# Kernel tuning notes

Hardware: AMD Instinct MI355X
Metric: run time of the kernel (lower is better)

The kernel has to match this reference:

```python
import jax, jax.numpy as jnp
import numpy as np

K = 3          # kernel_size
STRIDE_H = 1
STRIDE_W = 1


def setup_inputs() -> dict:
    key = jax.random.key(0)
    k1, k2, k3, k4 = jax.random.split(key, 4)
    inputs = jax.random.normal(k1, (8, 128, 128, 128), dtype=jnp.float32)
    weight = jax.random.normal(k2, (128, 128, K, K), dtype=jnp.float32) * 0.05
    # learned per-image rate map, fractional dilations in [1, 3)
    rates = jax.random.uniform(k3, (1, 1, 32, 32), dtype=jnp.float32) * 2.0 + 1.0
    bias = jax.random.normal(k4, (128,), dtype=jnp.float32) * 0.01
    return {"inputs": inputs, "weight": weight, "rates": rates, "bias": bias}


def _interp_bilinear(r, out_h, out_w):
    # torch F.interpolate(mode='bilinear', align_corners=False) on a 2D map r[in_h,in_w]
    in_h, in_w = r.shape
    def src(n_out, n_in):
        s = (jnp.arange(n_out, dtype=jnp.float32) + 0.5) * (n_in / n_out) - 0.5
        return jnp.clip(s, 0.0, n_in - 1.0)
    sy = src(out_h, in_h)
    sx = src(out_w, in_w)
    y0 = jnp.floor(sy).astype(jnp.int32)
    x0 = jnp.floor(sx).astype(jnp.int32)
    y1 = jnp.minimum(y0 + 1, in_h - 1)
    x1 = jnp.minimum(x0 + 1, in_w - 1)
    wy = (sy - y0.astype(jnp.float32))[:, None]   # [out_h,1]
    wx = (sx - x0.astype(jnp.float32))[None, :]   # [1,out_w]
    return (r[y0[:, None], x0[None, :]] * (1 - wy) * (1 - wx)
            + r[y0[:, None], x1[None, :]] * (1 - wy) * wx
            + r[y1[:, None], x0[None, :]] * wy * (1 - wx)
            + r[y1[:, None], x1[None, :]] * wy * wx)


def _bilinear_sample(img, y, x):
    # img: [N,C,H,W]; y,x: [Ho,Wo] float positions; zero padding outside.
    H, W = img.shape[2], img.shape[3]
    y0 = jnp.floor(y).astype(jnp.int32)
    x0 = jnp.floor(x).astype(jnp.int32)
    y1, x1 = y0 + 1, x0 + 1
    wy = y - y0.astype(img.dtype)
    wx = x - x0.astype(img.dtype)
    def tap(yi, xi):
        m = ((yi >= 0) & (yi < H) & (xi >= 0) & (xi < W)).astype(img.dtype)
        yc = jnp.clip(yi, 0, H - 1)
        xc = jnp.clip(xi, 0, W - 1)
        return img[:, :, yc, xc] * m  # [N,C,Ho,Wo]
    return (tap(y0, x0) * (1 - wy) * (1 - wx)
            + tap(y0, x1) * (1 - wy) * wx
            + tap(y1, x0) * wy * (1 - wx)
            + tap(y1, x1) * wy * wx)


def reference(inputs, weight, rates, bias):
    N, Cin, H, W = inputs.shape
    Ho = (H - K) // STRIDE_H + 1
    Wo = (W - K) // STRIDE_W + 1
    rate = _interp_bilinear(rates[0, 0], Ho, Wo)          # [Ho,Wo]
    base_y = jnp.arange(Ho, dtype=jnp.float32)[:, None] * STRIDE_H
    base_x = jnp.arange(Wo, dtype=jnp.float32)[None, :] * STRIDE_W
    out = jnp.broadcast_to(bias[None, :, None, None], (N, weight.shape[0], Ho, Wo)).astype(inputs.dtype)
    # fixed K*K = 9 taps; each tap samples the input at p0 + k*rate (per-pixel dilation)
    for kh in range(K):
        for kw in range(K):
            y = base_y + kh * rate
            x = base_x + kw * rate
            samp = _bilinear_sample(inputs, y, x)          # [N,Cin,Ho,Wo]
            out = out + jnp.einsum('oc,nchw->nohw', weight[:, :, kh, kw], samp)
    return out
```

## Files before the change

### kernel.cpp

```cpp
#include <hip/hip_runtime.h>
#include <hip/hip_fp16.h>

#define N_    8
#define CIN   128
#define COUT  128
#define H_    128
#define W_    128
#define HO    126
#define WO    126
#define PIXPER (HO*WO)
#define TOTPIX (N_*PIXPER)
#define PT    128
#define BLKPERIMG 125
#define NBLK  (N_*BLKPERIMG)

typedef _Float16 f16x8 __attribute__((ext_vector_type(8)));
typedef _Float16 f16x4 __attribute__((ext_vector_type(4)));
typedef float    f32x4 __attribute__((ext_vector_type(4)));

union U4H {
    uint4   u;
    __half2 h[4];
    f16x8   f;
};

#define GLLDS(gp, lp) __builtin_amdgcn_global_load_lds( \
    (const __attribute__((address_space(1))) unsigned int*)(gp), \
    (__attribute__((address_space(3))) unsigned int*)(lp), 16, 0, 0)

__global__ __launch_bounds__(256) void transpose_in_kernel(
    const float* __restrict__ in, _Float16* __restrict__ in_cl)
{
    __shared__ float tile[64][65];
    int bid = blockIdx.x;
    int hwt = bid & 255;
    int ct  = (bid >> 8) & 1;
    int n   = bid >> 9;
    int r0  = threadIdx.x >> 4;
    int c4  = (threadIdx.x & 15) * 4;
    const float* src = in + ((size_t)(n * CIN + ct * 64) * 16384) + hwt * 64;
#pragma unroll
    for (int k = 0; k < 4; ++k) {
        int row = r0 + k * 16;
        float4 v = *(const float4*)(src + (size_t)row * 16384 + c4);
        *(float4*)&tile[row][c4] = v;
    }
    __syncthreads();
    _Float16* dst = in_cl + ((size_t)(n * 16384 + hwt * 64) * 128) + ct * 64;
#pragma unroll
    for (int k = 0; k < 4; ++k) {
        int hw = r0 + k * 16;
        f16x4 o;
        o[0] = (_Float16)tile[c4 + 0][hw];
        o[1] = (_Float16)tile[c4 + 1][hw];
        o[2] = (_Float16)tile[c4 + 2][hw];
        o[3] = (_Float16)tile[c4 + 3][hw];
        *(f16x4*)(dst + (size_t)hw * 128 + c4) = o;
    }
}

__global__ void transpose_w_kernel(const float* __restrict__ w, _Float16* __restrict__ wt) {
    int t = blockIdx.x * 256 + threadIdx.x;
    int o = t >> 7, c = t & 127;
    int g = c >> 3;
    int dst = (((o << 4) | (g ^ (o & 7))) << 3) | (c & 7);
    const float* s = w + (size_t)(o * 128 + c) * 9;
#pragma unroll
    for (int tap = 0; tap < 9; ++tap)
        wt[tap * 16384 + dst] = (_Float16)s[tap];
}

__device__ __forceinline__ void gather_issue(
    int KH, int KW, U4H (&G)[4][4], int j0, int grp, int gl, unsigned nbase,
    const _Float16* __restrict__ in_cl,
    const int (*sPYi)[PT], const int (*sPXi)[PT])
{
    const unsigned lo = (unsigned)(gl * 8);
#pragma unroll
    for (int jj = 0; jj < 4; ++jj) {
        int px = grp * 8 + j0 + jj;
        int y0 = sPYi[KH][px];
        int x0 = sPXi[KW][px];
        int yc0 = min(y0, H_ - 1), yc1 = min(y0 + 1, H_ - 1);
        int xc0 = min(x0, W_ - 1), xc1 = min(x0 + 1, W_ - 1);
        G[jj][0].u = *(const uint4*)(in_cl + (((nbase + (unsigned)(yc0 * W_ + xc0)) << 7) + lo));
        if (KW != 0)
            G[jj][1].u = *(const uint4*)(in_cl + (((nbase + (unsigned)(yc0 * W_ + xc1)) << 7) + lo));
        if (KH != 0)
            G[jj][2].u = *(const uint4*)(in_cl + (((nbase + (unsigned)(yc1 * W_ + xc0)) << 7) + lo));
        if (KH != 0 && KW != 0)
            G[jj][3].u = *(const uint4*)(in_cl + (((nbase + (unsigned)(yc1 * W_ + xc1)) << 7) + lo));
    }
}

__device__ __forceinline__ void gather_lerp_store(
    int KH, int KW, U4H (&G)[4][4], int j0, int grp, int gl,
    _Float16* sS,
    const int (*sPYi)[PT], const float (*sPYf)[PT],
    const int (*sPXi)[PT], const float (*sPXf)[PT])
{
#pragma unroll
    for (int jj = 0; jj < 4; ++jj) {
        int j  = j0 + jj;
        int px = grp * 8 + j;
        U4H S;
        if (KH == 0 && KW == 0) {
            S = G[jj][0];
        } else {
            int   y0 = sPYi[KH][px];  float wy = sPYf[KH][px];
            int   x0 = sPXi[KW][px];  float wx = sPXf[KW][px];
            float vy0 = (y0 <= H_ - 1) ? 1.0f : 0.0f;
            float vy1 = (y0 <= H_ - 2) ? 1.0f : 0.0f;
            float vx0 = (x0 <= W_ - 1) ? 1.0f : 0.0f;
            float vx1 = (x0 <= W_ - 2) ? 1.0f : 0.0f;
            __half2 w00 = __float2half2_rn((1.0f - wy) * (1.0f - wx) * vy0 * vx0);
            __half2 w01 = __float2half2_rn((1.0f - wy) * wx * vy0 * vx1);
            __half2 w10 = __float2half2_rn(wy * (1.0f - wx) * vy1 * vx0);
            __half2 w11 = __float2half2_rn(wy * wx * vy1 * vx1);
#pragma unroll
            for (int d = 0; d < 4; ++d) {
                __half2 s = __hmul2(G[jj][0].h[d], w00);
                if (KW != 0)              s = __hfma2(G[jj][1].h[d], w01, s);
                if (KH != 0)              s = __hfma2(G[jj][2].h[d], w10, s);
                if (KH != 0 && KW != 0)   s = __hfma2(G[jj][3].h[d], w11, s);
                S.h[d] = s;
            }
        }
        *(f16x8*)&sS[px * 128 + ((unsigned)(gl ^ j)) * 8] = S.f;
    }
}

__global__ __launch_bounds__(256, 2) void adc_main(
    const _Float16* __restrict__ in_cl, const _Float16* __restrict__ wt,
    const float* __restrict__ rates, const float* __restrict__ bias,
    float* __restrict__ out)
{
    __shared__ uint4    sW[2048];
    __shared__ __align__(16) _Float16 sS[PT * 128];
    __shared__ int      sPYi[3][PT];
    __shared__ float    sPYf[3][PT];
    __shared__ int      sPXi[3][PT];
    __shared__ float    sPXf[3][PT];

    const int t    = threadIdx.x;
    const int lane = t & 63;
    const int wv   = t >> 6;
    const int l15  = lane & 15;
    const int quad = lane >> 4;

    const int n     = blockIdx.x & 7;
    const int pbase = (blockIdx.x >> 3) * PT;
    const unsigned nbase = (unsigned)n << 14;

    if (t < PT) {
        int rem = min(pbase + t, PIXPER - 1);
        int ho = rem / WO, wo = rem - ho * WO;
        const float sc = 32.0f / 126.0f;
        float sy = fminf(fmaxf(((float)ho + 0.5f) * sc - 0.5f, 0.0f), 31.0f);
        float sx = fminf(fmaxf(((float)wo + 0.5f) * sc - 0.5f, 0.0f), 31.0f);
        int y0 = (int)sy, x0 = (int)sx;
        int y1 = min(y0 + 1, 31), x1 = min(x0 + 1, 31);
        float wy = sy - (float)y0, wx = sx - (float)x0;
        float r = rates[y0 * 32 + x0] * (1.0f - wy) * (1.0f - wx)
                + rates[y0 * 32 + x1] * (1.0f - wy) * wx
                + rates[y1 * 32 + x0] * wy * (1.0f - wx)
                + rates[y1 * 32 + x1] * wy * wx;
#pragma unroll
        for (int k = 0; k < 3; ++k) {
            float fy  = (float)ho + (float)k * r;
            float fy0 = floorf(fy);
            sPYi[k][t] = (int)fy0;
            sPYf[k][t] = fy - fy0;
            float fx  = (float)wo + (float)k * r;
            float fx0 = floorf(fx);
            sPXi[k][t] = (int)fx0;
            sPXf[k][t] = fx - fx0;
        }
    }

    f32x4 acc[8][2];
    const f32x4 zero = {0.0f, 0.0f, 0.0f, 0.0f};
#pragma unroll
    for (int i = 0; i < 8; ++i) { acc[i][0] = zero; acc[i][1] = zero; }

    const int grp = t >> 4;
    const int gl  = t & 15;

    __syncthreads();

    U4H G[4][4];

    gather_issue(0, 0, G, 0, grp, gl, nbase, in_cl, sPYi, sPXi);

#pragma unroll
    for (int tap = 0; tap < 9; ++tap) {
        const int kh = tap / 3;
        const int kw = tap - kh * 3;

        const uint4* wsrc = (const uint4*)(wt + tap * 16384);
#pragma unroll
        for (int i = 0; i < 8; ++i) {
            int base = i * 256 + (wv << 6);
            GLLDS(wsrc + base + lane, &sW[base]);
        }

        gather_lerp_store(kh, kw, G, 0, grp, gl, sS, sPYi, sPYf, sPXi, sPXf);
        gather_issue(kh, kw, G, 4, grp, gl, nbase, in_cl, sPYi, sPXi);
        gather_lerp_store(kh, kw, G, 4, grp, gl, sS, sPYi, sPYf, sPXi, sPXf);

        __syncthreads();

        if (tap < 8) {
            const int tap1 = tap + 1;
            const int kh1 = tap1 / 3;
            const int kw1 = tap1 - kh1 * 3;
            gather_issue(kh1, kw1, G, 0, grp, gl, nbase, in_cl, sPYi, sPXi);
        }

#pragma unroll
        for (int ks = 0; ks < 4; ++ks) {
            const int g  = (ks << 2) | quad;
            const int sw = g ^ (l15 & 7);
            f16x8 b0 = *(const f16x8*)&sS[(wv * 32 +      l15) * 128 + sw * 8];
            f16x8 b1 = *(const f16x8*)&sS[(wv * 32 + 16 + l15) * 128 + sw * 8];
#pragma unroll
            for (int mt = 0; mt < 8; ++mt) {
                int o = (mt << 4) | l15;
                U4H AF;
                AF.u = sW[(o << 4) | sw];
                acc[mt][0] = __builtin_amdgcn_mfma_f32_16x16x32_f16(AF.f, b0, acc[mt][0], 0, 0, 0);
                acc[mt][1] = __builtin_amdgcn_mfma_f32_16x16x32_f16(AF.f, b1, acc[mt][1], 0, 0, 0);
            }
        }
        __syncthreads();
    }

#pragma unroll
    for (int pt = 0; pt < 2; ++pt) {
        int p    = (wv << 5) + (pt << 4) + l15;
        int prel = pbase + p;
        int rem2 = min(prel, PIXPER - 1);
        float* obase = out + (size_t)n * (COUT * PIXPER) + rem2;
        if (prel < PIXPER) {
#pragma unroll
            for (int mt = 0; mt < 8; ++mt) {
                int o0 = (mt << 4) + (quad << 2);
                float4 bs = *(const float4*)(bias + o0);
                f32x4 a0 = acc[mt][pt];
                obase[(size_t)(o0 + 0) * PIXPER] = a0[0] + bs.x;
                obase[(size_t)(o0 + 1) * PIXPER] = a0[1] + bs.y;
                obase[(size_t)(o0 + 2) * PIXPER] = a0[2] + bs.z;
                obase[(size_t)(o0 + 3) * PIXPER] = a0[3] + bs.w;
            }
        }
    }
}

extern "C" void kernel_launch(void* const* d_in, const int* in_sizes, int n_in,
                              void* d_out, int out_size, void* d_ws, size_t ws_size,
                              hipStream_t stream) {
    const float* inputs = (const float*)d_in[0];
    const float* weight = (const float*)d_in[1];
    const float* rates  = (const float*)d_in[2];
    const float* bias   = (const float*)d_in[3];
    float* out = (float*)d_out;

    char* ws = (char*)d_ws;
    _Float16* in_cl = (_Float16*)ws;
    _Float16* wtp   = (_Float16*)(ws + 33554432);

    transpose_w_kernel<<<64, 256, 0, stream>>>(weight, wtp);
    transpose_in_kernel<<<4096, 256, 0, stream>>>(inputs, in_cl);
    adc_main<<<NBLK, 256, 0, stream>>>(in_cl, wtp, rates, bias, out);
}
```

Before: 186.3 us.

## Read MFMA weights from global in fragment layout and precompute bilinear tap weights

Drops the per-tap LDS staging of weights. The weights are pre-permuted so each lane's MFMA A fragment is one contiguous 16-byte global load served from cache. The bilinear corner weights for all 9 taps are precomputed once per pixel as packed halves in shared memory, which removes the per-tap float math. Freeing LDS and registers raises launch_bounds occupancy to 3 blocks per CU. In exchange, the cross-tap gather prefetch is removed, so gather latency is now exposed, and weight reads go through L1/L2 on every MFMA step.

```diff
diff --git a/kernel.cpp b/kernel.cpp
--- a/kernel.cpp
+++ b/kernel.cpp
@@ -23,10 +23,10 @@
     __half2 h[4];
     f16x8   f;
 };
-
-#define GLLDS(gp, lp) __builtin_amdgcn_global_load_lds( \
-    (const __attribute__((address_space(1))) unsigned int*)(gp), \
-    (__attribute__((address_space(3))) unsigned int*)(lp), 16, 0, 0)
+union U2H {
+    uint2  u;
+    __half h[4];
+};
 
 __global__ __launch_bounds__(256) void transpose_in_kernel(
     const float* __restrict__ in, _Float16* __restrict__ in_cl)
@@ -62,12 +62,15 @@
 __global__ void transpose_w_kernel(const float* __restrict__ w, _Float16* __restrict__ wt) {
     int t = blockIdx.x * 256 + threadIdx.x;
     int o = t >> 7, c = t & 127;
-    int g = c >> 3;
-    int dst = (((o << 4) | (g ^ (o & 7))) << 3) | (c & 7);
+    int mt = o >> 4, l15 = o & 15;
+    int ks = c >> 5, quad = (c >> 3) & 3, d = c & 7;
+    int lane = (quad << 4) | l15;
     const float* s = w + (size_t)(o * 128 + c) * 9;
 #pragma unroll
-    for (int tap = 0; tap < 9; ++tap)
-        wt[tap * 16384 + dst] = (_Float16)s[tap];
+    for (int tap = 0; tap < 9; ++tap) {
+        int idx = ((((tap * 8 + mt) * 4 + ks) << 6) + lane) * 8 + d;
+        wt[idx] = (_Float16)s[tap];
+    }
 }
 
 __device__ __forceinline__ void gather_issue(
@@ -94,10 +97,8 @@
 }
 
 __device__ __forceinline__ void gather_lerp_store(
-    int KH, int KW, U4H (&G)[4][4], int j0, int grp, int gl,
-    _Float16* sS,
-    const int (*sPYi)[PT], const float (*sPYf)[PT],
-    const int (*sPXi)[PT], const float (*sPXf)[PT])
+    int TAP, int KH, int KW, U4H (&G)[4][4], int j0, int grp, int gl,
+    _Float16* sS, const uint2 (*sPW)[PT])
 {
 #pragma unroll
     for (int jj = 0; jj < 4; ++jj) {
@@ -107,16 +108,12 @@
         if (KH == 0 && KW == 0) {
             S = G[jj][0];
         } else {
-            int   y0 = sPYi[KH][px];  float wy = sPYf[KH][px];
-            int   x0 = sPXi[KW][px];  float wx = sPXf[KW][px];
-            float vy0 = (y0 <= H_ - 1) ? 1.0f : 0.0f;
-            float vy1 = (y0 <= H_ - 2) ? 1.0f : 0.0f;
-            float vx0 = (x0 <= W_ - 1) ? 1.0f : 0.0f;
-            float vx1 = (x0 <= W_ - 2) ? 1.0f : 0.0f;
-            __half2 w00 = __float2half2_rn((1.0f - wy) * (1.0f - wx) * vy0 * vx0);
-            __half2 w01 = __float2half2_rn((1.0f - wy) * wx * vy0 * vx1);
-            __half2 w10 = __float2half2_rn(wy * (1.0f - wx) * vy1 * vx0);
-            __half2 w11 = __float2half2_rn(wy * wx * vy1 * vx1);
+            U2H W4;
+            W4.u = sPW[TAP][px];
+            __half2 w00 = __half2half2(W4.h[0]);
+            __half2 w01 = __half2half2(W4.h[1]);
+            __half2 w10 = __half2half2(W4.h[2]);
+            __half2 w11 = __half2half2(W4.h[3]);
 #pragma unroll
             for (int d = 0; d < 4; ++d) {
                 __half2 s = __hmul2(G[jj][0].h[d], w00);
@@ -130,17 +127,15 @@
     }
 }
 
-__global__ __launch_bounds__(256, 2) void adc_main(
-    const _Float16* __restrict__ in_cl, const _Float16* __restrict__ wt,
+__global__ __launch_bounds__(256, 3) void adc_main(
+    const _Float16* __restrict__ in_cl, const _Float16* __restrict__ wtA,
     const float* __restrict__ rates, const float* __restrict__ bias,
     float* __restrict__ out)
 {
-    __shared__ uint4    sW[2048];
     __shared__ __align__(16) _Float16 sS[PT * 128];
-    __shared__ int      sPYi[3][PT];
-    __shared__ float    sPYf[3][PT];
-    __shared__ int      sPXi[3][PT];
-    __shared__ float    sPXf[3][PT];
+    __shared__ uint2 sPW[9][PT];
+    __shared__ int   sPYi[3][PT];
+    __shared__ int   sPXi[3][PT];
 
     const int t    = threadIdx.x;
     const int lane = t & 63;
@@ -158,24 +153,42 @@
         const float sc = 32.0f / 126.0f;
         float sy = fminf(fmaxf(((float)ho + 0.5f) * sc - 0.5f, 0.0f), 31.0f);
         float sx = fminf(fmaxf(((float)wo + 0.5f) * sc - 0.5f, 0.0f), 31.0f);
-        int y0 = (int)sy, x0 = (int)sx;
-        int y1 = min(y0 + 1, 31), x1 = min(x0 + 1, 31);
-        float wy = sy - (float)y0, wx = sx - (float)x0;
-        float r = rates[y0 * 32 + x0] * (1.0f - wy) * (1.0f - wx)
-                + rates[y0 * 32 + x1] * (1.0f - wy) * wx
-                + rates[y1 * 32 + x0] * wy * (1.0f - wx)
-                + rates[y1 * 32 + x1] * wy * wx;
+        int y0r = (int)sy, x0r = (int)sx;
+        int y1r = min(y0r + 1, 31), x1r = min(x0r + 1, 31);
+        float wyr = sy - (float)y0r, wxr = sx - (float)x0r;
+        float r = rates[y0r * 32 + x0r] * (1.0f - wyr) * (1.0f - wxr)
+                + rates[y0r * 32 + x1r] * (1.0f - wyr) * wxr
+                + rates[y1r * 32 + x0r] * wyr * (1.0f - wxr)
+                + rates[y1r * 32 + x1r] * wyr * wxr;
+        float hy0[3], hy1[3], hx0[3], hx1[3];
 #pragma unroll
         for (int k = 0; k < 3; ++k) {
             float fy  = (float)ho + (float)k * r;
             float fy0 = floorf(fy);
-            sPYi[k][t] = (int)fy0;
-            sPYf[k][t] = fy - fy0;
+            int   y0  = (int)fy0;
+            float wy  = fy - fy0;
+            sPYi[k][t] = y0;
+            hy0[k] = (1.0f - wy) * ((y0 <= H_ - 1) ? 1.0f : 0.0f);
+            hy1[k] = wy          * ((y0 <= H_ - 2) ? 1.0f : 0.0f);
             float fx  = (float)wo + (float)k * r;
             float fx0 = floorf(fx);
-            sPXi[k][t] = (int)fx0;
-            sPXf[k][t] = fx - fx0;
-        }
+            int   x0  = (int)fx0;
+            float wx  = fx - fx0;
+            sPXi[k][t] = x0;
+            hx0[k] = (1.0f - wx) * ((x0 <= W_ - 1) ? 1.0f : 0.0f);
+            hx1[k] = wx          * ((x0 <= W_ - 2) ? 1.0f : 0.0f);
+        }
+#pragma unroll
+        for (int kh = 0; kh < 3; ++kh)
+#pragma unroll
+            for (int kw = 0; kw < 3; ++kw) {
+                U2H W4;
+                W4.h[0] = __float2half(hy0[kh] * hx0[kw]);
+                W4.h[1] = __float2half(hy0[kh] * hx1[kw]);
+                W4.h[2] = __float2half(hy1[kh] * hx0[kw]);
+                W4.h[3] = __float2half(hy1[kh] * hx1[kw]);
+                sPW[kh * 3 + kw][t] = W4.u;
+            }
     }
 
     f32x4 acc[8][2];
@@ -186,50 +199,35 @@
     const int grp = t >> 4;
     const int gl  = t & 15;
 
+    const _Float16* wbase = wtA + lane * 8;
+
     __syncthreads();
-
-    U4H G[4][4];
-
-    gather_issue(0, 0, G, 0, grp, gl, nbase, in_cl, sPYi, sPXi);
 
 #pragma unroll
     for (int tap = 0; tap < 9; ++tap) {
         const int kh = tap / 3;
         const int kw = tap - kh * 3;
 
-        const uint4* wsrc = (const uint4*)(wt + tap * 16384);
-#pragma unroll
-        for (int i = 0; i < 8; ++i) {
-            int base = i * 256 + (wv << 6);
-            GLLDS(wsrc + base + lane, &sW[base]);
-        }
-
-        gather_lerp_store(kh, kw, G, 0, grp, gl, sS, sPYi, sPYf, sPXi, sPXf);
-        gather_issue(kh, kw, G, 4, grp, gl, nbase, in_cl, sPYi, sPXi);
-        gather_lerp_store(kh, kw, G, 4, grp, gl, sS, sPYi, sPYf, sPXi, sPXf);
-
+        {
+            U4H G[4][4];
+            gather_issue(kh, kw, G, 0, grp, gl, nbase, in_cl, sPYi, sPXi);
+            gather_lerp_store(tap, kh, kw, G, 0, grp, gl, sS, sPW);
+            gather_issue(kh, kw, G, 4, grp, gl, nbase, in_cl, sPYi, sPXi);
+            gather_lerp_store(tap, kh, kw, G, 4, grp, gl, sS, sPW);
+        }
         __syncthreads();
 
-        if (tap < 8) {
-            const int tap1 = tap + 1;
-            const int kh1 = tap1 / 3;
-            const int kw1 = tap1 - kh1 * 3;
-            gather_issue(kh1, kw1, G, 0, grp, gl, nbase, in_cl, sPYi, sPXi);
-        }
-
+        const _Float16* wtap = wbase + tap * 16384;
 #pragma unroll
         for (int ks = 0; ks < 4; ++ks) {
-            const int g  = (ks << 2) | quad;
-            const int sw = g ^ (l15 & 7);
+            const int sw = ((ks << 2) | quad) ^ (l15 & 7);
             f16x8 b0 = *(const f16x8*)&sS[(wv * 32 +      l15) * 128 + sw * 8];
             f16x8 b1 = *(const f16x8*)&sS[(wv * 32 + 16 + l15) * 128 + sw * 8];
 #pragma unroll
             for (int mt = 0; mt < 8; ++mt) {
-                int o = (mt << 4) | l15;
-                U4H AF;
-                AF.u = sW[(o << 4) | sw];
-                acc[mt][0] = __builtin_amdgcn_mfma_f32_16x16x32_f16(AF.f, b0, acc[mt][0], 0, 0, 0);
-                acc[mt][1] = __builtin_amdgcn_mfma_f32_16x16x32_f16(AF.f, b1, acc[mt][1], 0, 0, 0);
+                f16x8 AF = *(const f16x8*)(wtap + mt * 2048 + ks * 512);
+                acc[mt][0] = __builtin_amdgcn_mfma_f32_16x16x32_f16(AF, b0, acc[mt][0], 0, 0, 0);
+                acc[mt][1] = __builtin_amdgcn_mfma_f32_16x16x32_f16(AF, b1, acc[mt][1], 0, 0, 0);
             }
         }
         __syncthreads();
```

Measured after the change: 230.4 us. 1.24x slower.
